# Optimization experiments

Measured on AMD Instinct MI355X. Metric: run time of the kernel, lower is better.

The kernel has to match this reference:

```python
import jax, jax.numpy as jnp
import numpy as np

N_NODES = 100000
N_EDGES = 3200000
HIDDEN = 64


def _gcn_conv(x, W, b, row, col, norm, n_nodes):
    # x: [N, Fin] -> [N, Fout]; symmetric-normalized scatter-add aggregation
    xw = x @ W  # [N, Fout]
    msg = xw[row] * norm[:, None]  # [E', Fout] gather + scale
    out = jax.ops.segment_sum(msg, col, num_segments=n_nodes)  # scatter-add
    return out + b


def _norm_and_loops(edge_index, n_nodes):
    # add self loops (PyG GCNConv default) and compute D^-1/2 norm per edge
    loops = jnp.arange(n_nodes, dtype=edge_index.dtype)
    row = jnp.concatenate([edge_index[0], loops])
    col = jnp.concatenate([edge_index[1], loops])
    deg = jax.ops.segment_sum(jnp.ones_like(col, dtype=jnp.float32), col,
                              num_segments=n_nodes)
    dis = jnp.where(deg > 0, 1.0 / jnp.sqrt(deg), 0.0)
    norm = dis[row] * dis[col]
    return row, col, norm


def setup_inputs() -> dict:
    key = jax.random.key(0)
    k1, k2, k3, k4 = jax.random.split(key, 4)
    x = jax.random.normal(k1, (N_NODES, 1), dtype=jnp.float32)
    edge_index = jax.random.randint(k2, (2, N_EDGES), 0, N_NODES, dtype=jnp.int64)
    # Glorot-ish init for GCN weights
    W1 = jax.random.normal(k3, (1, HIDDEN), dtype=jnp.float32) * (1.0 / np.sqrt(1))
    b1 = jnp.zeros((HIDDEN,), dtype=jnp.float32)
    W2 = jax.random.normal(k4, (HIDDEN, 1), dtype=jnp.float32) * (1.0 / np.sqrt(HIDDEN))
    b2 = jnp.zeros((1,), dtype=jnp.float32)
    return {"x": x, "edge_index": edge_index, "W1": W1, "b1": b1, "W2": W2, "b2": b2}


def reference(x, edge_index, W1, b1, W2, b2):
    n = x.shape[0]
    row, col, norm = _norm_and_loops(edge_index, n)
    h = _gcn_conv(x, W1, b1, row, col, norm, n)   # [N, 64]
    out = _gcn_conv(h, W2, b2, row, col, norm, n)  # [N, 1]
    return out
```

## Files before the change

kernel.cpp:

```cpp
#include <hip/hip_runtime.h>
#include <math.h>


#define CHUNK 256
#define CHUNK_SHIFT 8
#define PACK_SHIFT 17
#define ROW_MASK ((1u << PACK_SHIFT) - 1u)
#define NBMAX 512
#define SLICES 256
#define CAPB 80
#define CAPB_V (CAPB / 4)
#define TPB 512
#define PLACE_TPB 1024

static __device__ __forceinline__ int gid() {
    return blockIdx.x * blockDim.x + threadIdx.x;
}

__global__ void __launch_bounds__(PLACE_TPB)
k_place(const int* __restrict__ row, const int* __restrict__ col,
        int E, int NB, int* __restrict__ len, unsigned* __restrict__ sorted) {
    __shared__ int cnt[NBMAX];
    const int tid = threadIdx.x;
    const int blk = blockIdx.x;
    for (int t = tid; t < NB; t += PLACE_TPB) cnt[t] = 0;
    __syncthreads();
    int quads = E >> 2;
    int per = (quads + gridDim.x - 1) / gridDim.x;
    int qlo = blk * per, qhi = min(quads, qlo + per);
    for (int q = qlo + tid; q < qhi; q += PLACE_TPB) {
        int4 r = reinterpret_cast<const int4*>(row)[q];
        int4 c = reinterpret_cast<const int4*>(col)[q];
        {
            int b = c.x >> CHUNK_SHIFT;
            int i = atomicAdd(&cnt[b], 1);
            if (i < CAPB)
                sorted[((size_t)b * SLICES + blk) * CAPB + i] =
                    (unsigned)r.x | ((unsigned)(c.x & (CHUNK - 1)) << PACK_SHIFT);
        }
        {
            int b = c.y >> CHUNK_SHIFT;
            int i = atomicAdd(&cnt[b], 1);
            if (i < CAPB)
                sorted[((size_t)b * SLICES + blk) * CAPB + i] =
                    (unsigned)r.y | ((unsigned)(c.y & (CHUNK - 1)) << PACK_SHIFT);
        }
        {
            int b = c.z >> CHUNK_SHIFT;
            int i = atomicAdd(&cnt[b], 1);
            if (i < CAPB)
                sorted[((size_t)b * SLICES + blk) * CAPB + i] =
                    (unsigned)r.z | ((unsigned)(c.z & (CHUNK - 1)) << PACK_SHIFT);
        }
        {
            int b = c.w >> CHUNK_SHIFT;
            int i = atomicAdd(&cnt[b], 1);
            if (i < CAPB)
                sorted[((size_t)b * SLICES + blk) * CAPB + i] =
                    (unsigned)r.w | ((unsigned)(c.w & (CHUNK - 1)) << PACK_SHIFT);
        }
    }
    if (blk == 0 && tid == 0) {
        for (int j = quads << 2; j < E; ++j) {
            int cc = col[j];
            int b = cc >> CHUNK_SHIFT;
            int i = atomicAdd(&cnt[b], 1);
            if (i < CAPB)
                sorted[((size_t)b * SLICES) * CAPB + i] =
                    (unsigned)row[j] | ((unsigned)(cc & (CHUNK - 1)) << PACK_SHIFT);
        }
    }
    __syncthreads();
    for (int t = tid; t < NB; t += PLACE_TPB)
        len[(size_t)t * SLICES + blk] = min(cnt[t], CAPB);
}


__global__ void __launch_bounds__(TPB)
k_acc1(const unsigned* __restrict__ sorted, const int* __restrict__ len,
       const float* __restrict__ x, float* __restrict__ dis, float* __restrict__ g,
       int N) {
    __shared__ float acc[CHUNK];
    __shared__ int slen[SLICES];
    const int b = blockIdx.x;
    const int tid = threadIdx.x;
    if (tid < CHUNK) acc[tid] = 0.0f;
    for (int t = tid; t < SLICES; t += TPB) slen[t] = len[(size_t)b * SLICES + t];
    __syncthreads();
    const uint4* bs = reinterpret_cast<const uint4*>(sorted + (size_t)b * SLICES * CAPB);
    const int TOTV = SLICES * CAPB_V;
    for (int j = tid; j < TOTV; j += TPB) {
        int s = j / CAPB_V;
        int l = slen[s];
        int base = (j - s * CAPB_V) << 2;
        if (base >= l) continue;
        uint4 p = bs[j];
        atomicAdd(&acc[p.x >> PACK_SHIFT], 1.0f);
        if (base + 1 < l) atomicAdd(&acc[p.y >> PACK_SHIFT], 1.0f);
        if (base + 2 < l) atomicAdd(&acc[p.z >> PACK_SHIFT], 1.0f);
        if (base + 3 < l) atomicAdd(&acc[p.w >> PACK_SHIFT], 1.0f);
    }
    __syncthreads();
    int i = b * CHUNK + tid;
    if (tid < CHUNK && i < N) {
        float d = rsqrtf(1.0f + acc[tid]);
        dis[i] = d;
        g[i] = d * x[i];
    }
}

__global__ void __launch_bounds__(TPB)
k_acc2(const unsigned* __restrict__ sorted, const int* __restrict__ len,
       const float* __restrict__ g, const float* __restrict__ dis,
       const float* __restrict__ W1, const float* __restrict__ b1,
       const float* __restrict__ W2, int H,
       float* __restrict__ g2, int N) {
    __shared__ float acc[CHUNK];
    __shared__ int slen[SLICES];
    __shared__ float sab[2];
    const int b = blockIdx.x;
    const int tid = threadIdx.x;
    if (tid < CHUNK) acc[tid] = 0.0f;
    for (int t = tid; t < SLICES; t += TPB) slen[t] = len[(size_t)b * SLICES + t];
    if (tid >= CHUNK && tid < CHUNK + 64) {
        int t = tid - CHUNK;
        float w2 = (t < H) ? W2[t] : 0.0f;
        float a = (t < H) ? W1[t] * w2 : 0.0f;
        float bb = (t < H) ? b1[t] * w2 : 0.0f;
        for (int o = 32; o; o >>= 1) {
            a += __shfl_down(a, o, 64);
            bb += __shfl_down(bb, o, 64);
        }
        if (t == 0) { sab[0] = a; sab[1] = bb; }
    }
    __syncthreads();
    const uint4* bs = reinterpret_cast<const uint4*>(sorted + (size_t)b * SLICES * CAPB);
    const int TOTV = SLICES * CAPB_V;
    for (int j = tid; j < TOTV; j += TPB) {
        int s = j / CAPB_V;
        int l = slen[s];
        int base = (j - s * CAPB_V) << 2;
        if (base >= l) continue;
        uint4 p = bs[j];
        atomicAdd(&acc[p.x >> PACK_SHIFT], g[p.x & ROW_MASK]);
        if (base + 1 < l) atomicAdd(&acc[p.y >> PACK_SHIFT], g[p.y & ROW_MASK]);
        if (base + 2 < l) atomicAdd(&acc[p.z >> PACK_SHIFT], g[p.z & ROW_MASK]);
        if (base + 3 < l) atomicAdd(&acc[p.w >> PACK_SHIFT], g[p.w & ROW_MASK]);
    }
    __syncthreads();
    int i = b * CHUNK + tid;
    if (tid < CHUNK && i < N) {
        float d = dis[i];
        float s = d * (g[i] + acc[tid]);
        g2[i] = d * (sab[0] * s + sab[1]);
    }
}

__global__ void __launch_bounds__(TPB)
k_acc3(const unsigned* __restrict__ sorted, const int* __restrict__ len,
       const float* __restrict__ g2, const float* __restrict__ dis,
       const float* __restrict__ b2, float* __restrict__ out, int N) {
    __shared__ float acc[CHUNK];
    __shared__ int slen[SLICES];
    const int b = blockIdx.x;
    const int tid = threadIdx.x;
    if (tid < CHUNK) acc[tid] = 0.0f;
    for (int t = tid; t < SLICES; t += TPB) slen[t] = len[(size_t)b * SLICES + t];
    __syncthreads();
    const uint4* bs = reinterpret_cast<const uint4*>(sorted + (size_t)b * SLICES * CAPB);
    const int TOTV = SLICES * CAPB_V;
    for (int j = tid; j < TOTV; j += TPB) {
        int s = j / CAPB_V;
        int l = slen[s];
        int base = (j - s * CAPB_V) << 2;
        if (base >= l) continue;
        uint4 p = bs[j];
        atomicAdd(&acc[p.x >> PACK_SHIFT], g2[p.x & ROW_MASK]);
        if (base + 1 < l) atomicAdd(&acc[p.y >> PACK_SHIFT], g2[p.y & ROW_MASK]);
        if (base + 2 < l) atomicAdd(&acc[p.z >> PACK_SHIFT], g2[p.z & ROW_MASK]);
        if (base + 3 < l) atomicAdd(&acc[p.w >> PACK_SHIFT], g2[p.w & ROW_MASK]);
    }
    __syncthreads();
    int i = b * CHUNK + tid;
    if (tid < CHUNK && i < N)
        out[i] = dis[i] * (g2[i] + acc[tid]) + b2[0];
}


__global__ void k_zero_f(float* __restrict__ p, int n) {
    int i = gid();
    if (i < n) p[i] = 0.0f;
}

__global__ void k_ab_fb(const float* __restrict__ W1, const float* __restrict__ b1,
                        const float* __restrict__ W2, float* __restrict__ ab, int hidden) {
    int t = threadIdx.x;
    float w2 = (t < hidden) ? W2[t] : 0.0f;
    float a = (t < hidden) ? W1[t] * w2 : 0.0f;
    float b = (t < hidden) ? b1[t] * w2 : 0.0f;
    for (int o = 32; o; o >>= 1) {
        a += __shfl_down(a, o, 64);
        b += __shfl_down(b, o, 64);
    }
    if (t == 0) { ab[0] = a; ab[1] = b; }
}

__global__ void k_deg_fb(const int* __restrict__ col, float* __restrict__ t, int E) {
    int i = gid();
    if (i < E) atomicAdd(&t[col[i]], 1.0f);
}

__global__ void k_scat_fb(const int* __restrict__ ei, const float* __restrict__ val,
                          float* __restrict__ t, int E) {
    int i = gid();
    if (i < E) atomicAdd(&t[ei[E + i]], val[ei[i]]);
}

__global__ void k_node1_fb(const float* __restrict__ x, const float* __restrict__ degsum,
                           float* __restrict__ dis, float* __restrict__ g, int N) {
    int i = gid();
    if (i < N) {
        float d = rsqrtf(1.0f + degsum[i]);
        dis[i] = d;
        g[i] = d * x[i];
    }
}

__global__ void k_node2_fb(const float* __restrict__ g, const float* __restrict__ dis,
                           const float* __restrict__ ab, const float* __restrict__ sum1,
                           float* __restrict__ g2, int N) {
    int i = gid();
    if (i < N) {
        float s = dis[i] * (g[i] + sum1[i]);
        g2[i] = dis[i] * (ab[0] * s + ab[1]);
    }
}

__global__ void k_node3_fb(const float* __restrict__ g2, const float* __restrict__ dis,
                           const float* __restrict__ b2, const float* __restrict__ sum2,
                           float* __restrict__ out, int N) {
    int i = gid();
    if (i < N) out[i] = dis[i] * (g2[i] + sum2[i]) + b2[0];
}

extern "C" void kernel_launch(void* const* d_in, const int* in_sizes, int n_in,
                              void* d_out, int out_size, void* d_ws, size_t ws_size,
                              hipStream_t stream) {
    const float* x  = (const float*)d_in[0];
    const int*   ei = (const int*)d_in[1];
    const float* W1 = (const float*)d_in[2];
    const float* b1 = (const float*)d_in[3];
    const float* W2 = (const float*)d_in[4];
    const float* b2 = (const float*)d_in[5];
    float* out = (float*)d_out;

    const int N = in_sizes[0];
    const int E = in_sizes[1] / 2;
    const int H = in_sizes[2];
    const int NB = (N + CHUNK - 1) >> CHUNK_SHIFT;

    const int slice_mean = (E / SLICES) / (NB > 0 ? NB : 1);

    char* w = (char*)d_ws;
    unsigned* sorted = (unsigned*)w;   w += (size_t)NB * SLICES * CAPB * 4;
    int* len = (int*)w;                w += (size_t)NB * SLICES * 4;
    float* dis = (float*)w;            w += (size_t)N * 4;
    float* g   = (float*)w;            w += (size_t)N * 4;
    float* g2  = (float*)w;            w += (size_t)N * 4;
    size_t needed = (size_t)(w - (char*)d_ws);

    const int BLK = 256;
    const int nodeGrid = (N + BLK - 1) / BLK;

    if (N <= (1 << PACK_SHIFT) && NB <= NBMAX && H <= 64 &&
        slice_mean * 2 <= CAPB && ws_size >= needed) {
        k_place<<<SLICES, PLACE_TPB, 0, stream>>>(ei, ei + E, E, NB, len, sorted);
        k_acc1<<<NB, TPB, 0, stream>>>(sorted, len, x, dis, g, N);
        k_acc2<<<NB, TPB, 0, stream>>>(sorted, len, g, dis, W1, b1, W2, H, g2, N);
        k_acc3<<<NB, TPB, 0, stream>>>(sorted, len, g2, dis, b2, out, N);
    } else {
        float* fdis = (float*)d_ws;
        float* fg   = fdis + N;
        float* fg2  = fg + N;
        float* ftmp = fg2 + N;
        float* fab  = ftmp + N;
        const int eGrid = (E + BLK - 1) / BLK;
        k_ab_fb<<<1, 64, 0, stream>>>(W1, b1, W2, fab, H);
        k_zero_f<<<nodeGrid, BLK, 0, stream>>>(ftmp, N);
        k_deg_fb<<<eGrid, BLK, 0, stream>>>(ei + E, ftmp, E);
        k_node1_fb<<<nodeGrid, BLK, 0, stream>>>(x, ftmp, fdis, fg, N);
        k_zero_f<<<nodeGrid, BLK, 0, stream>>>(ftmp, N);
        k_scat_fb<<<eGrid, BLK, 0, stream>>>(ei, fg, ftmp, E);
        k_node2_fb<<<nodeGrid, BLK, 0, stream>>>(fg, fdis, fab, ftmp, fg2, N);
        k_zero_f<<<nodeGrid, BLK, 0, stream>>>(ftmp, N);
        k_scat_fb<<<eGrid, BLK, 0, stream>>>(ei, fg2, ftmp, E);
        k_node3_fb<<<nodeGrid, BLK, 0, stream>>>(fg2, fdis, b2, ftmp, out, N);
    }
}
```

Baseline: 102.1 us.

## Stage edges and row-group tiles of node values in LDS for aggregation

In the second and third aggregation kernels, each block first compacts its packed edges into a shared-memory edge buffer using a prefix scan over the per-slice lengths. It then walks the source-node range in groups of 8192 rows. For each group it loads that slice of the node-value array into LDS and accumulates only the edges whose source falls in it. This replaces random global gathers with coalesced tile loads and LDS lookups. The cost is that every block reads the whole value array, makes about 13 passes over its edges with barriers in between, and uses roughly 70KB of LDS, which cuts occupancy. Edges beyond the 9216-entry buffer would be silently dropped.

New measurement: 226.5 us. 2.22x slower.

```diff
diff --git a/kernel.cpp b/kernel.cpp
--- a/kernel.cpp
+++ b/kernel.cpp
@@ -12,6 +12,10 @@
 #define CAPB_V (CAPB / 4)
 #define TPB 512
 #define PLACE_TPB 1024
+#define RG_BITS 13
+#define RG_SIZE (1 << RG_BITS)
+#define RG_MASK (RG_SIZE - 1)
+#define EBUF_CAP 9216
 
 static __device__ __forceinline__ int gid() {
     return blockIdx.x * blockDim.x + threadIdx.x;
@@ -74,7 +78,6 @@
     for (int t = tid; t < NB; t += PLACE_TPB)
         len[(size_t)t * SLICES + blk] = min(cnt[t], CAPB);
 }
-
 
 __global__ void __launch_bounds__(TPB)
 k_acc1(const unsigned* __restrict__ sorted, const int* __restrict__ len,
@@ -109,19 +112,73 @@
     }
 }
 
+
+static __device__ __forceinline__ void
+acc_staged(const unsigned* __restrict__ sorted, const int* __restrict__ len,
+           const float* __restrict__ val, int RG_CNT, int b, int tid,
+           unsigned* ebuf, float* gstage, int* slen, int* soff, float* acc, int N) {
+    if (tid < CHUNK) acc[tid] = 0.0f;
+    for (int t = tid; t < SLICES; t += TPB) slen[t] = len[(size_t)b * SLICES + t];
+    __syncthreads();
+    if (tid < SLICES) soff[tid] = slen[tid];
+    __syncthreads();
+    for (int off = 1; off < SLICES; off <<= 1) {
+        int v = 0;
+        if (tid < SLICES) {
+            v = soff[tid];
+            if (tid >= off) v += soff[tid - off];
+        }
+        __syncthreads();
+        if (tid < SLICES) soff[tid] = v;
+        __syncthreads();
+    }
+    const uint4* bs = reinterpret_cast<const uint4*>(sorted + (size_t)b * SLICES * CAPB);
+    const int TOTV = SLICES * CAPB_V;
+    for (int j = tid; j < TOTV; j += TPB) {
+        int s = j / CAPB_V;
+        int l = slen[s];
+        int base = (j - s * CAPB_V) << 2;
+        if (base >= l) continue;
+        uint4 p = bs[j];
+        int e0 = soff[s] - l + base;
+        if (e0 < EBUF_CAP) ebuf[e0] = p.x;
+        if (base + 1 < l && e0 + 1 < EBUF_CAP) ebuf[e0 + 1] = p.y;
+        if (base + 2 < l && e0 + 2 < EBUF_CAP) ebuf[e0 + 2] = p.z;
+        if (base + 3 < l && e0 + 3 < EBUF_CAP) ebuf[e0 + 3] = p.w;
+    }
+    __syncthreads();
+    int blen = min(soff[SLICES - 1], EBUF_CAP);
+    for (int rg = 0; rg < RG_CNT; ++rg) {
+        int rbase = rg << RG_BITS;
+        for (int t = tid; t < RG_SIZE; t += TPB) {
+            int r = rbase + t;
+            gstage[t] = (r < N) ? val[r] : 0.0f;
+        }
+        __syncthreads();
+        for (int j = tid; j < blen; j += TPB) {
+            unsigned e = ebuf[j];
+            unsigned r = e & ROW_MASK;
+            if ((int)(r >> RG_BITS) == rg)
+                atomicAdd(&acc[e >> PACK_SHIFT], gstage[r & RG_MASK]);
+        }
+        __syncthreads();
+    }
+}
+
 __global__ void __launch_bounds__(TPB)
 k_acc2(const unsigned* __restrict__ sorted, const int* __restrict__ len,
        const float* __restrict__ g, const float* __restrict__ dis,
        const float* __restrict__ W1, const float* __restrict__ b1,
-       const float* __restrict__ W2, int H,
+       const float* __restrict__ W2, int H, int RG_CNT,
        float* __restrict__ g2, int N) {
+    __shared__ unsigned ebuf[EBUF_CAP];
+    __shared__ float gstage[RG_SIZE];
+    __shared__ int slen[SLICES];
+    __shared__ int soff[SLICES];
     __shared__ float acc[CHUNK];
-    __shared__ int slen[SLICES];
     __shared__ float sab[2];
     const int b = blockIdx.x;
     const int tid = threadIdx.x;
-    if (tid < CHUNK) acc[tid] = 0.0f;
-    for (int t = tid; t < SLICES; t += TPB) slen[t] = len[(size_t)b * SLICES + t];
     if (tid >= CHUNK && tid < CHUNK + 64) {
         int t = tid - CHUNK;
         float w2 = (t < H) ? W2[t] : 0.0f;
@@ -133,21 +190,7 @@
         }
         if (t == 0) { sab[0] = a; sab[1] = bb; }
     }
-    __syncthreads();
-    const uint4* bs = reinterpret_cast<const uint4*>(sorted + (size_t)b * SLICES * CAPB);
-    const int TOTV = SLICES * CAPB_V;
-    for (int j = tid; j < TOTV; j += TPB) {
-        int s = j / CAPB_V;
-        int l = slen[s];
-        int base = (j - s * CAPB_V) << 2;
-        if (base >= l) continue;
-        uint4 p = bs[j];
-        atomicAdd(&acc[p.x >> PACK_SHIFT], g[p.x & ROW_MASK]);
-        if (base + 1 < l) atomicAdd(&acc[p.y >> PACK_SHIFT], g[p.y & ROW_MASK]);
-        if (base + 2 < l) atomicAdd(&acc[p.z >> PACK_SHIFT], g[p.z & ROW_MASK]);
-        if (base + 3 < l) atomicAdd(&acc[p.w >> PACK_SHIFT], g[p.w & ROW_MASK]);
-    }
-    __syncthreads();
+    acc_staged(sorted, len, g, RG_CNT, b, tid, ebuf, gstage, slen, soff, acc, N);
     int i = b * CHUNK + tid;
     if (tid < CHUNK && i < N) {
         float d = dis[i];
@@ -159,28 +202,15 @@
 __global__ void __launch_bounds__(TPB)
 k_acc3(const unsigned* __restrict__ sorted, const int* __restrict__ len,
        const float* __restrict__ g2, const float* __restrict__ dis,
-       const float* __restrict__ b2, float* __restrict__ out, int N) {
+       const float* __restrict__ b2, int RG_CNT, float* __restrict__ out, int N) {
+    __shared__ unsigned ebuf[EBUF_CAP];
+    __shared__ float gstage[RG_SIZE];
+    __shared__ int slen[SLICES];
+    __shared__ int soff[SLICES];
     __shared__ float acc[CHUNK];
-    __shared__ int slen[SLICES];
     const int b = blockIdx.x;
     const int tid = threadIdx.x;
-    if (tid < CHUNK) acc[tid] = 0.0f;
-    for (int t = tid; t < SLICES; t += TPB) slen[t] = len[(size_t)b * SLICES + t];
-    __syncthreads();
-    const uint4* bs = reinterpret_cast<const uint4*>(sorted + (size_t)b * SLICES * CAPB);
-    const int TOTV = SLICES * CAPB_V;
-    for (int j = tid; j < TOTV; j += TPB) {
-        int s = j / CAPB_V;
-        int l = slen[s];
-        int base = (j - s * CAPB_V) << 2;
-        if (base >= l) continue;
-        uint4 p = bs[j];
-        atomicAdd(&acc[p.x >> PACK_SHIFT], g2[p.x & ROW_MASK]);
-        if (base + 1 < l) atomicAdd(&acc[p.y >> PACK_SHIFT], g2[p.y & ROW_MASK]);
-        if (base + 2 < l) atomicAdd(&acc[p.z >> PACK_SHIFT], g2[p.z & ROW_MASK]);
-        if (base + 3 < l) atomicAdd(&acc[p.w >> PACK_SHIFT], g2[p.w & ROW_MASK]);
-    }
-    __syncthreads();
+    acc_staged(sorted, len, g2, RG_CNT, b, tid, ebuf, gstage, slen, soff, acc, N);
     int i = b * CHUNK + tid;
     if (tid < CHUNK && i < N)
         out[i] = dis[i] * (g2[i] + acc[tid]) + b2[0];
@@ -258,6 +288,7 @@
     const int E = in_sizes[1] / 2;
     const int H = in_sizes[2];
     const int NB = (N + CHUNK - 1) >> CHUNK_SHIFT;
+    const int RG_CNT = (N + RG_SIZE - 1) >> RG_BITS;
 
     const int slice_mean = (E / SLICES) / (NB > 0 ? NB : 1);
 
@@ -272,12 +303,12 @@
     const int BLK = 256;
     const int nodeGrid = (N + BLK - 1) / BLK;
 
-    if (N <= (1 << PACK_SHIFT) && NB <= NBMAX && H <= 64 &&
+    if (N <= (1 << PACK_SHIFT) && NB <= NBMAX && H <= 64 && RG_CNT <= 16 &&
         slice_mean * 2 <= CAPB && ws_size >= needed) {
         k_place<<<SLICES, PLACE_TPB, 0, stream>>>(ei, ei + E, E, NB, len, sorted);
         k_acc1<<<NB, TPB, 0, stream>>>(sorted, len, x, dis, g, N);
-        k_acc2<<<NB, TPB, 0, stream>>>(sorted, len, g, dis, W1, b1, W2, H, g2, N);
-        k_acc3<<<NB, TPB, 0, stream>>>(sorted, len, g2, dis, b2, out, N);
+        k_acc2<<<NB, TPB, 0, stream>>>(sorted, len, g, dis, W1, b1, W2, H, RG_CNT, g2, N);
+        k_acc3<<<NB, TPB, 0, stream>>>(sorted, len, g2, dis, b2, RG_CNT, out, N);
     } else {
         float* fdis = (float*)d_ws;
         float* fg   = fdis + N;
```

## Stage bucketed edges in shared memory before coalesced global write

Applied to the files above, without the earlier changes.

The placement kernel now runs a counting pass over the columns, takes a prefix sum of the bucket counts in shared memory, and scatters the packed edges into a shared-memory staging buffer. Each wavefront then copies whole buckets contiguously to global memory. This replaces scattered per-edge global stores with coalesced writes, at the cost of reading the column array twice and adding several block-wide synchronisations for the scan. A host-side guard ensures the per-slice edge count fits the staging buffer.

After: 94.30 us. -7.7%, faster.

```diff
diff --git a/kernel.cpp b/kernel.cpp
--- a/kernel.cpp
+++ b/kernel.cpp
@@ -12,6 +12,7 @@
 #define CAPB_V (CAPB / 4)
 #define TPB 512
 #define PLACE_TPB 1024
+#define STAGE_CAP 12544
 
 static __device__ __forceinline__ int gid() {
     return blockIdx.x * blockDim.x + threadIdx.x;
@@ -20,59 +21,89 @@
 __global__ void __launch_bounds__(PLACE_TPB)
 k_place(const int* __restrict__ row, const int* __restrict__ col,
         int E, int NB, int* __restrict__ len, unsigned* __restrict__ sorted) {
+    __shared__ unsigned stage[STAGE_CAP];
     __shared__ int cnt[NBMAX];
+    __shared__ int soff[NBMAX];
+    __shared__ int wcnt[NBMAX];
     const int tid = threadIdx.x;
     const int blk = blockIdx.x;
-    for (int t = tid; t < NB; t += PLACE_TPB) cnt[t] = 0;
-    __syncthreads();
     int quads = E >> 2;
     int per = (quads + gridDim.x - 1) / gridDim.x;
     int qlo = blk * per, qhi = min(quads, qlo + per);
+
+    for (int t = tid; t < NBMAX; t += PLACE_TPB) { cnt[t] = 0; wcnt[t] = 0; }
+    __syncthreads();
+
+    for (int q = qlo + tid; q < qhi; q += PLACE_TPB) {
+        int4 c = reinterpret_cast<const int4*>(col)[q];
+        atomicAdd(&cnt[c.x >> CHUNK_SHIFT], 1);
+        atomicAdd(&cnt[c.y >> CHUNK_SHIFT], 1);
+        atomicAdd(&cnt[c.z >> CHUNK_SHIFT], 1);
+        atomicAdd(&cnt[c.w >> CHUNK_SHIFT], 1);
+    }
+    if (blk == 0 && tid == 0)
+        for (int j = quads << 2; j < E; ++j)
+            atomicAdd(&cnt[col[j] >> CHUNK_SHIFT], 1);
+    __syncthreads();
+
+    if (tid < NBMAX) soff[tid] = cnt[tid];
+    __syncthreads();
+    for (int o = 1; o < NBMAX; o <<= 1) {
+        int v = 0;
+        if (tid < NBMAX) {
+            v = soff[tid];
+            if (tid >= o) v += soff[tid - o];
+        }
+        __syncthreads();
+        if (tid < NBMAX) soff[tid] = v;
+        __syncthreads();
+    }
+    if (tid < NBMAX) soff[tid] -= cnt[tid];
+    __syncthreads();
+
     for (int q = qlo + tid; q < qhi; q += PLACE_TPB) {
         int4 r = reinterpret_cast<const int4*>(row)[q];
         int4 c = reinterpret_cast<const int4*>(col)[q];
         {
             int b = c.x >> CHUNK_SHIFT;
-            int i = atomicAdd(&cnt[b], 1);
-            if (i < CAPB)
-                sorted[((size_t)b * SLICES + blk) * CAPB + i] =
-                    (unsigned)r.x | ((unsigned)(c.x & (CHUNK - 1)) << PACK_SHIFT);
+            int p = soff[b] + atomicAdd(&wcnt[b], 1);
+            stage[p] = (unsigned)r.x | ((unsigned)(c.x & (CHUNK - 1)) << PACK_SHIFT);
         }
         {
             int b = c.y >> CHUNK_SHIFT;
-            int i = atomicAdd(&cnt[b], 1);
-            if (i < CAPB)
-                sorted[((size_t)b * SLICES + blk) * CAPB + i] =
-                    (unsigned)r.y | ((unsigned)(c.y & (CHUNK - 1)) << PACK_SHIFT);
+            int p = soff[b] + atomicAdd(&wcnt[b], 1);
+            stage[p] = (unsigned)r.y | ((unsigned)(c.y & (CHUNK - 1)) << PACK_SHIFT);
         }
         {
             int b = c.z >> CHUNK_SHIFT;
-            int i = atomicAdd(&cnt[b], 1);
-            if (i < CAPB)
-                sorted[((size_t)b * SLICES + blk) * CAPB + i] =
-                    (unsigned)r.z | ((unsigned)(c.z & (CHUNK - 1)) << PACK_SHIFT);
+            int p = soff[b] + atomicAdd(&wcnt[b], 1);
+            stage[p] = (unsigned)r.z | ((unsigned)(c.z & (CHUNK - 1)) << PACK_SHIFT);
         }
         {
             int b = c.w >> CHUNK_SHIFT;
-            int i = atomicAdd(&cnt[b], 1);
-            if (i < CAPB)
-                sorted[((size_t)b * SLICES + blk) * CAPB + i] =
-                    (unsigned)r.w | ((unsigned)(c.w & (CHUNK - 1)) << PACK_SHIFT);
+            int p = soff[b] + atomicAdd(&wcnt[b], 1);
+            stage[p] = (unsigned)r.w | ((unsigned)(c.w & (CHUNK - 1)) << PACK_SHIFT);
         }
     }
     if (blk == 0 && tid == 0) {
         for (int j = quads << 2; j < E; ++j) {
             int cc = col[j];
             int b = cc >> CHUNK_SHIFT;
-            int i = atomicAdd(&cnt[b], 1);
-            if (i < CAPB)
-                sorted[((size_t)b * SLICES) * CAPB + i] =
-                    (unsigned)row[j] | ((unsigned)(cc & (CHUNK - 1)) << PACK_SHIFT);
-        }
-    }
-    __syncthreads();
-    for (int t = tid; t < NB; t += PLACE_TPB)
-        len[(size_t)t * SLICES + blk] = min(cnt[t], CAPB);
+            int p = soff[b] + atomicAdd(&wcnt[b], 1);
+            stage[p] = (unsigned)row[j] | ((unsigned)(cc & (CHUNK - 1)) << PACK_SHIFT);
+        }
+    }
+    __syncthreads();
+
+    const int wid = tid >> 6, lane = tid & 63;
+    const int nw = PLACE_TPB >> 6;
+    for (int b = wid; b < NB; b += nw) {
+        int c = min(cnt[b], CAPB);
+        int lb = soff[b];
+        unsigned* dst = sorted + ((size_t)b * SLICES + blk) * CAPB;
+        for (int i = lane; i < c; i += 64) dst[i] = stage[lb + i];
+        if (lane == 0) len[(size_t)b * SLICES + blk] = c;
+    }
 }
 
 
@@ -259,6 +290,9 @@
     const int H = in_sizes[2];
     const int NB = (N + CHUNK - 1) >> CHUNK_SHIFT;
 
+    const int per_quads = ((E >> 2) + SLICES - 1) / SLICES;
+    const int stage_need = per_quads * 4 + 8;
+
     const int slice_mean = (E / SLICES) / (NB > 0 ? NB : 1);
 
     char* w = (char*)d_ws;
@@ -273,7 +307,7 @@
     const int nodeGrid = (N + BLK - 1) / BLK;
 
     if (N <= (1 << PACK_SHIFT) && NB <= NBMAX && H <= 64 &&
-        slice_mean * 2 <= CAPB && ws_size >= needed) {
+        stage_need <= STAGE_CAP && slice_mean * 2 <= CAPB && ws_size >= needed) {
         k_place<<<SLICES, PLACE_TPB, 0, stream>>>(ei, ei + E, E, NB, len, sorted);
         k_acc1<<<NB, TPB, 0, stream>>>(sorted, len, x, dis, g, N);
         k_acc2<<<NB, TPB, 0, stream>>>(sorted, len, g, dis, W1, b1, W2, H, g2, N);
```

## Stage bucketed edges in LDS before coalesced write-out; widen accumulation blocks

Applied to the files above, without the earlier changes.

k_place now gathers its packed edges in a 128KB shared-memory staging buffer, one region per bucket. Once all edges are placed, each wavefront copies whole buckets to global memory with contiguous stores, replacing the scattered per-edge global writes. The three accumulation kernels move from 512 to 1024 threads per block and unroll their loop by two to expose more memory-level parallelism. The large LDS footprint limits k_place to one block per CU, and the bucket limit drops to 400.

New measurement: 90.20 us. -11.7%, faster.

```diff
diff --git a/kernel.cpp b/kernel.cpp
--- a/kernel.cpp
+++ b/kernel.cpp
@@ -7,10 +7,11 @@
 #define PACK_SHIFT 17
 #define ROW_MASK ((1u << PACK_SHIFT) - 1u)
 #define NBMAX 512
+#define NBP 400
 #define SLICES 256
 #define CAPB 80
 #define CAPB_V (CAPB / 4)
-#define TPB 512
+#define ATPB 1024
 #define PLACE_TPB 1024
 
 static __device__ __forceinline__ int gid() {
@@ -20,11 +21,13 @@
 __global__ void __launch_bounds__(PLACE_TPB)
 k_place(const int* __restrict__ row, const int* __restrict__ col,
         int E, int NB, int* __restrict__ len, unsigned* __restrict__ sorted) {
-    __shared__ int cnt[NBMAX];
+    __shared__ unsigned stage[NBP * CAPB];
+    __shared__ int cnt[NBP];
     const int tid = threadIdx.x;
     const int blk = blockIdx.x;
     for (int t = tid; t < NB; t += PLACE_TPB) cnt[t] = 0;
     __syncthreads();
+
     int quads = E >> 2;
     int per = (quads + gridDim.x - 1) / gridDim.x;
     int qlo = blk * per, qhi = min(quads, qlo + per);
@@ -35,28 +38,28 @@
             int b = c.x >> CHUNK_SHIFT;
             int i = atomicAdd(&cnt[b], 1);
             if (i < CAPB)
-                sorted[((size_t)b * SLICES + blk) * CAPB + i] =
+                stage[b * CAPB + i] =
                     (unsigned)r.x | ((unsigned)(c.x & (CHUNK - 1)) << PACK_SHIFT);
         }
         {
             int b = c.y >> CHUNK_SHIFT;
             int i = atomicAdd(&cnt[b], 1);
             if (i < CAPB)
-                sorted[((size_t)b * SLICES + blk) * CAPB + i] =
+                stage[b * CAPB + i] =
                     (unsigned)r.y | ((unsigned)(c.y & (CHUNK - 1)) << PACK_SHIFT);
         }
         {
             int b = c.z >> CHUNK_SHIFT;
             int i = atomicAdd(&cnt[b], 1);
             if (i < CAPB)
-                sorted[((size_t)b * SLICES + blk) * CAPB + i] =
+                stage[b * CAPB + i] =
                     (unsigned)r.z | ((unsigned)(c.z & (CHUNK - 1)) << PACK_SHIFT);
         }
         {
             int b = c.w >> CHUNK_SHIFT;
             int i = atomicAdd(&cnt[b], 1);
             if (i < CAPB)
-                sorted[((size_t)b * SLICES + blk) * CAPB + i] =
+                stage[b * CAPB + i] =
                     (unsigned)r.w | ((unsigned)(c.w & (CHUNK - 1)) << PACK_SHIFT);
         }
     }
@@ -66,17 +69,24 @@
             int b = cc >> CHUNK_SHIFT;
             int i = atomicAdd(&cnt[b], 1);
             if (i < CAPB)
-                sorted[((size_t)b * SLICES) * CAPB + i] =
+                stage[b * CAPB + i] =
                     (unsigned)row[j] | ((unsigned)(cc & (CHUNK - 1)) << PACK_SHIFT);
         }
     }
     __syncthreads();
-    for (int t = tid; t < NB; t += PLACE_TPB)
-        len[(size_t)t * SLICES + blk] = min(cnt[t], CAPB);
-}
-
-
-__global__ void __launch_bounds__(TPB)
+
+    const int wid = tid >> 6, lane = tid & 63;
+    const int nw = PLACE_TPB >> 6;
+    for (int b = wid; b < NB; b += nw) {
+        int c = min(cnt[b], CAPB);
+        unsigned* dst = sorted + ((size_t)b * SLICES + blk) * CAPB;
+        for (int i = lane; i < c; i += 64) dst[i] = stage[b * CAPB + i];
+        if (lane == 0) len[(size_t)b * SLICES + blk] = c;
+    }
+}
+
+
+__global__ void __launch_bounds__(ATPB)
 k_acc1(const unsigned* __restrict__ sorted, const int* __restrict__ len,
        const float* __restrict__ x, float* __restrict__ dis, float* __restrict__ g,
        int N) {
@@ -85,11 +95,12 @@
     const int b = blockIdx.x;
     const int tid = threadIdx.x;
     if (tid < CHUNK) acc[tid] = 0.0f;
-    for (int t = tid; t < SLICES; t += TPB) slen[t] = len[(size_t)b * SLICES + t];
+    for (int t = tid; t < SLICES; t += ATPB) slen[t] = len[(size_t)b * SLICES + t];
     __syncthreads();
     const uint4* bs = reinterpret_cast<const uint4*>(sorted + (size_t)b * SLICES * CAPB);
     const int TOTV = SLICES * CAPB_V;
-    for (int j = tid; j < TOTV; j += TPB) {
+    #pragma unroll 2
+    for (int j = tid; j < TOTV; j += ATPB) {
         int s = j / CAPB_V;
         int l = slen[s];
         int base = (j - s * CAPB_V) << 2;
@@ -109,7 +120,7 @@
     }
 }
 
-__global__ void __launch_bounds__(TPB)
+__global__ void __launch_bounds__(ATPB)
 k_acc2(const unsigned* __restrict__ sorted, const int* __restrict__ len,
        const float* __restrict__ g, const float* __restrict__ dis,
        const float* __restrict__ W1, const float* __restrict__ b1,
@@ -121,7 +132,7 @@
     const int b = blockIdx.x;
     const int tid = threadIdx.x;
     if (tid < CHUNK) acc[tid] = 0.0f;
-    for (int t = tid; t < SLICES; t += TPB) slen[t] = len[(size_t)b * SLICES + t];
+    for (int t = tid; t < SLICES; t += ATPB) slen[t] = len[(size_t)b * SLICES + t];
     if (tid >= CHUNK && tid < CHUNK + 64) {
         int t = tid - CHUNK;
         float w2 = (t < H) ? W2[t] : 0.0f;
@@ -136,7 +147,8 @@
     __syncthreads();
     const uint4* bs = reinterpret_cast<const uint4*>(sorted + (size_t)b * SLICES * CAPB);
     const int TOTV = SLICES * CAPB_V;
-    for (int j = tid; j < TOTV; j += TPB) {
+    #pragma unroll 2
+    for (int j = tid; j < TOTV; j += ATPB) {
         int s = j / CAPB_V;
         int l = slen[s];
         int base = (j - s * CAPB_V) << 2;
@@ -156,7 +168,7 @@
     }
 }
 
-__global__ void __launch_bounds__(TPB)
+__global__ void __launch_bounds__(ATPB)
 k_acc3(const unsigned* __restrict__ sorted, const int* __restrict__ len,
        const float* __restrict__ g2, const float* __restrict__ dis,
        const float* __restrict__ b2, float* __restrict__ out, int N) {
@@ -165,11 +177,12 @@
     const int b = blockIdx.x;
     const int tid = threadIdx.x;
     if (tid < CHUNK) acc[tid] = 0.0f;
-    for (int t = tid; t < SLICES; t += TPB) slen[t] = len[(size_t)b * SLICES + t];
+    for (int t = tid; t < SLICES; t += ATPB) slen[t] = len[(size_t)b * SLICES + t];
     __syncthreads();
     const uint4* bs = reinterpret_cast<const uint4*>(sorted + (size_t)b * SLICES * CAPB);
     const int TOTV = SLICES * CAPB_V;
-    for (int j = tid; j < TOTV; j += TPB) {
+    #pragma unroll 2
+    for (int j = tid; j < TOTV; j += ATPB) {
         int s = j / CAPB_V;
         int l = slen[s];
         int base = (j - s * CAPB_V) << 2;
@@ -272,12 +285,12 @@
     const int BLK = 256;
     const int nodeGrid = (N + BLK - 1) / BLK;
 
-    if (N <= (1 << PACK_SHIFT) && NB <= NBMAX && H <= 64 &&
+    if (N <= (1 << PACK_SHIFT) && NB <= NBP && H <= 64 &&
         slice_mean * 2 <= CAPB && ws_size >= needed) {
         k_place<<<SLICES, PLACE_TPB, 0, stream>>>(ei, ei + E, E, NB, len, sorted);
-        k_acc1<<<NB, TPB, 0, stream>>>(sorted, len, x, dis, g, N);
-        k_acc2<<<NB, TPB, 0, stream>>>(sorted, len, g, dis, W1, b1, W2, H, g2, N);
-        k_acc3<<<NB, TPB, 0, stream>>>(sorted, len, g2, dis, b2, out, N);
+        k_acc1<<<NB, ATPB, 0, stream>>>(sorted, len, x, dis, g, N);
+        k_acc2<<<NB, ATPB, 0, stream>>>(sorted, len, g, dis, W1, b1, W2, H, g2, N);
+        k_acc3<<<NB, ATPB, 0, stream>>>(sorted, len, g2, dis, b2, out, N);
     } else {
         float* fdis = (float*)d_ws;
         float* fg   = fdis + N;
```
